# Kernel tuning notes

Measured on AMD Instinct MI355X. Metric: run time of the kernel, lower is better.

The kernel has to match this reference:

```python
import jax, jax.numpy as jnp
import numpy as np

B, N, M = 32, 65536, 64
IMG = 640.0
POS_THR, NEG_THR = 0.5, 0.4
ALPHA, GAMMA = 0.25, 2.0
BBOX_W = 2.0
EPS = 1e-6


def setup_inputs() -> dict:
    key = jax.random.key(0)
    k1, k2, k3, k4, k5 = jax.random.split(key, 5)
    # predictions: cx, cy in [0, IMG], w, h in [8, 72], obj logit ~ N(0,1)
    cxcy = jax.random.uniform(k1, (B, N, 2), jnp.float32) * IMG
    wh = jax.random.uniform(k2, (B, N, 2), jnp.float32) * 64.0 + 8.0
    obj = jax.random.normal(k3, (B, N, 1), jnp.float32)
    predictions = jnp.concatenate([cxcy, wh, obj], axis=-1)  # [B, N, 5]
    # ground-truth boxes in xyxy, centers in [0, IMG], sizes in [10, 100]
    gcxcy = jax.random.uniform(k4, (B, M, 2), jnp.float32) * IMG
    gwh = jax.random.uniform(k5, (B, M, 2), jnp.float32) * 90.0 + 10.0
    gt_boxes = jnp.concatenate([gcxcy - gwh / 2, gcxcy + gwh / 2], axis=-1)  # [B, M, 4]
    return {"predictions": predictions, "gt_boxes": gt_boxes}


def _focal(logits, targets):
    # stable BCE-with-logits, then focal modulation
    bce = jnp.maximum(logits, 0.0) - logits * targets + jnp.log1p(jnp.exp(-jnp.abs(logits)))
    p = jax.nn.sigmoid(logits)
    p_t = jnp.where(targets == 1.0, p, 1.0 - p)
    alpha_t = jnp.where(targets == 1.0, ALPHA, 1.0 - ALPHA)
    return alpha_t * (1.0 - p_t) ** GAMMA * bce


def _pairwise_iou(pb, gb):
    # pb: [N,4] xyxy, gb: [M,4] xyxy -> [N,M]
    x1 = jnp.maximum(pb[:, None, 0], gb[None, :, 0])
    y1 = jnp.maximum(pb[:, None, 1], gb[None, :, 1])
    x2 = jnp.minimum(pb[:, None, 2], gb[None, :, 2])
    y2 = jnp.minimum(pb[:, None, 3], gb[None, :, 3])
    inter = jnp.clip(x2 - x1, 0.0) * jnp.clip(y2 - y1, 0.0)
    area_p = (pb[:, 2] - pb[:, 0]) * (pb[:, 3] - pb[:, 1])
    area_g = (gb[:, 2] - gb[:, 0]) * (gb[:, 3] - gb[:, 1])
    union = area_p[:, None] + area_g[None, :] - inter
    return inter / jnp.clip(union, EPS)


def _giou_term(pb, gb):
    # elementwise 1 - GIoU; pb, gb: [N,4]
    x1 = jnp.maximum(pb[:, 0], gb[:, 0]); y1 = jnp.maximum(pb[:, 1], gb[:, 1])
    x2 = jnp.minimum(pb[:, 2], gb[:, 2]); y2 = jnp.minimum(pb[:, 3], gb[:, 3])
    inter = jnp.clip(x2 - x1, 0.0) * jnp.clip(y2 - y1, 0.0)
    area_p = (pb[:, 2] - pb[:, 0]) * (pb[:, 3] - pb[:, 1])
    area_g = (gb[:, 2] - gb[:, 0]) * (gb[:, 3] - gb[:, 1])
    union = area_p + area_g - inter
    iou = inter / jnp.clip(union, EPS)
    ex1 = jnp.minimum(pb[:, 0], gb[:, 0]); ey1 = jnp.minimum(pb[:, 1], gb[:, 1])
    ex2 = jnp.maximum(pb[:, 2], gb[:, 2]); ey2 = jnp.maximum(pb[:, 3], gb[:, 3])
    enc = (ex2 - ex1) * (ey2 - ey1)
    giou = iou - (enc - union) / jnp.clip(enc, EPS)
    return 1.0 - giou


def _per_image(pred, gt):
    # pred: [N,5] (cx,cy,w,h,obj), gt: [M,4] xyxy
    cx, cy, w, h = pred[:, 0], pred[:, 1], pred[:, 2], pred[:, 3]
    pb = jnp.stack([cx - w / 2, cy - h / 2, cx + w / 2, cy + h / 2], axis=1)  # decode to xyxy
    obj = pred[:, 4]
    ious = _pairwise_iou(pb, gt)  # [N, M]
    best_pred_per_gt = ious.max(axis=0)              # [M]
    best_pred_idx = jnp.argmax(ious, axis=0)         # [M]
    best_gt_per_pred = ious.max(axis=1)              # [N]
    best_gt_idx = jnp.argmax(ious, axis=1)           # [N]
    # force-match each GT's best anchor if its IoU > 0.1 (scatter-max)
    pos_scatter = jnp.zeros((pred.shape[0],), jnp.int32).at[best_pred_idx].max(
        (best_pred_per_gt > 0.1).astype(jnp.int32))
    pos = (pos_scatter > 0) | (best_gt_per_pred > POS_THR)
    neg = best_gt_per_pred < NEG_THR
    valid = pos | neg
    t = pos.astype(jnp.float32)
    fl = _focal(obj, t)
    vcnt = valid.sum().astype(jnp.float32)
    cls_loss = jnp.where(vcnt > 0, (fl * valid).sum() / jnp.maximum(vcnt, 1.0), 0.0)
    matched = gt[best_gt_idx]                        # [N,4]
    gterm = _giou_term(pb, matched)                  # [N]
    pcnt = pos.sum().astype(jnp.float32)
    reg_loss = jnp.where(pcnt > 0, (gterm * pos).sum() / jnp.maximum(pcnt, 1.0), 0.0)
    return cls_loss, reg_loss, pos.sum()


def reference(predictions, gt_boxes):
    cls_b, reg_b, npos_b = jax.vmap(_per_image)(predictions, gt_boxes)
    num_pos = jnp.maximum(npos_b.sum(), 1).astype(jnp.float32)
    bsz = jnp.float32(predictions.shape[0])
    total_cls = cls_b.sum() / bsz
    total_reg = reg_b.sum() / num_pos * bsz
    return total_cls + BBOX_W * total_reg
```

## Files before the change

### kernel.cpp

```cpp
#include <hip/hip_runtime.h>

#define NB 32
#define NPRED 65536
#define NGT 64
#define BLK 256
#define SLICES 32
#define CPB (NPRED / (SLICES * BLK))
#define NXB 32
#define BIN_SCALE 0.05f

#define POS_THR 0.5f
#define NEG_THR 0.4f
#define SCAT_THR 0.1f
#define EPSF 1e-6f


__device__ __forceinline__ int binidx(float x) {
    int bi = (int)(x * BIN_SCALE);
    return max(0, min(NXB - 1, bi));
}

__device__ __forceinline__ float focal_shared(float l, bool pos) {
    float e  = expf(-fabsf(l));
    float lg = log1pf(e);
    float rp = 1.f / (1.f + e);
    float p  = (l >= 0.f) ? rp : (1.f - rp);
    if (pos) { float q = 1.f - p; return 0.25f * q * q * ((fmaxf(l, 0.f) - l) + lg); }
    return 0.75f * p * p * (fmaxf(l, 0.f) + lg);
}

__device__ __forceinline__ float giou_term(float px1, float py1, float px2, float py2,
                                           float gx1, float gy1, float gx2, float gy2) {
    float x1 = fmaxf(px1, gx1), y1 = fmaxf(py1, gy1);
    float x2 = fminf(px2, gx2), y2 = fminf(py2, gy2);
    float dx = fmaxf(__fsub_rn(x2, x1), 0.f);
    float dy = fmaxf(__fsub_rn(y2, y1), 0.f);
    float inter = __fmul_rn(dx, dy);
    float ap = __fmul_rn(__fsub_rn(px2, px1), __fsub_rn(py2, py1));
    float ag = __fmul_rn(__fsub_rn(gx2, gx1), __fsub_rn(gy2, gy1));
    float uni = __fsub_rn(__fadd_rn(ap, ag), inter);
    float iou = __fdiv_rn(inter, fmaxf(uni, EPSF));
    float ex1 = fminf(px1, gx1), ey1 = fminf(py1, gy1);
    float ex2 = fmaxf(px2, gx2), ey2 = fmaxf(py2, gy2);
    float enc = __fmul_rn(__fsub_rn(ex2, ex1), __fsub_rn(ey2, ey1));
    float giou = __fsub_rn(iou, __fdiv_rn(__fsub_rn(enc, uni), fmaxf(enc, EPSF)));
    return __fsub_rn(1.f, giou);
}


__global__ __launch_bounds__(BLK) void passA(
    const float* __restrict__ pred, const float* __restrict__ gt,
    unsigned long long* __restrict__ keys,
    double* __restrict__ S_fl, double* __restrict__ S_gt,
    int* __restrict__ vcnt, int* __restrict__ pcnt)
{
    const int b = blockIdx.y;
    const int slice = blockIdx.x;
    const int tid = threadIdx.x;

    __shared__ float4 spred4[(BLK * 5) / 4];
    __shared__ float sgx1[NGT], sgy1[NGT], sgx2[NGT], sgy2[NGT], sgar[NGT];
    __shared__ unsigned long long skey[NGT];
    __shared__ unsigned long long binx[NXB], biny[NXB];
    __shared__ float rfl[BLK / 64], rgt[BLK / 64];
    __shared__ int rvp[BLK / 64];

    const float* base = pred + (size_t)b * NPRED * 5 + (size_t)slice * (CPB * BLK) * 5;

    const float4* src0 = (const float4*)base;
    float4 r0 = src0[tid];
    float4 r1;
    if (tid < 64) r1 = src0[BLK + tid];

    const float4* gtb = (const float4*)(gt + (size_t)b * NGT * 4);
    float4 gmine;
    if (tid < NGT) gmine = gtb[tid];
    if (tid < NXB) { binx[tid] = 0ULL; biny[tid] = 0ULL; }
    if (tid < NGT) {
        sgx1[tid] = gmine.x; sgy1[tid] = gmine.y;
        sgx2[tid] = gmine.z; sgy2[tid] = gmine.w;
        sgar[tid] = __fmul_rn(__fsub_rn(gmine.z, gmine.x), __fsub_rn(gmine.w, gmine.y));
        skey[tid] = 0ULL;
    }
    __syncthreads();
    if (tid < NGT) {
        unsigned long long bit = 1ULL << tid;
        int b1 = binidx(gmine.x), b2 = binidx(gmine.z);
        #pragma unroll
        for (int i = 0; i < 6; ++i) { int bb = min(b1 + i, NXB - 1); if (b1 + i <= b2) atomicOr(&binx[bb], bit); }
        b1 = binidx(gmine.y); b2 = binidx(gmine.w);
        #pragma unroll
        for (int i = 0; i < 6; ++i) { int bb = min(b1 + i, NXB - 1); if (b1 + i <= b2) atomicOr(&biny[bb], bit); }
    }

    float acc_fl = 0.f, acc_gt = 0.f;
    int acc_vp = 0;

    for (int c = 0; c < CPB; ++c) {
        __syncthreads();
        spred4[tid] = r0;
        if (tid < 64) spred4[BLK + tid] = r1;
        __syncthreads();
        if (c + 1 < CPB) {
            const float4* srcn = (const float4*)(base + (size_t)(c + 1) * BLK * 5);
            r0 = srcn[tid];
            if (tid < 64) r1 = srcn[BLK + tid];
        }

        const float* sp = (const float*)spred4;
        const float cx  = sp[tid * 5 + 0];
        const float cy  = sp[tid * 5 + 1];
        const float w   = sp[tid * 5 + 2];
        const float h   = sp[tid * 5 + 3];
        const float obj = sp[tid * 5 + 4];

        const float px1 = __fsub_rn(cx, __fmul_rn(w, 0.5f));
        const float py1 = __fsub_rn(cy, __fmul_rn(h, 0.5f));
        const float px2 = __fadd_rn(cx, __fmul_rn(w, 0.5f));
        const float py2 = __fadd_rn(cy, __fmul_rn(h, 0.5f));
        const float area_p = __fmul_rn(__fsub_rn(px2, px1), __fsub_rn(py2, py1));

        unsigned long long mx = 0ULL, my = 0ULL;
        {
            int b1 = binidx(px1), b2 = binidx(px2);
            #pragma unroll
            for (int i = 0; i < 5; ++i) { unsigned long long v = binx[min(b1 + i, NXB - 1)]; if (b1 + i <= b2) mx |= v; }
            b1 = binidx(py1); b2 = binidx(py2);
            #pragma unroll
            for (int i = 0; i < 5; ++i) { unsigned long long v = biny[min(b1 + i, NXB - 1)]; if (b1 + i <= b2) my |= v; }
        }
        unsigned long long m = mx & my;

        const unsigned n = (unsigned)(slice * (CPB * BLK) + c * BLK + tid);
        const unsigned long long nkey = (unsigned long long)(~n);

        float best_iou = 0.f;
        int best_j = 0;
        while (m) {
            int j0 = __ffsll(m) - 1; m &= m - 1;
            int j1 = -1;
            if (m) { j1 = __ffsll(m) - 1; m &= m - 1; }
            int j1c = (j1 >= 0) ? j1 : j0;
            float ax1 = sgx1[j0], ay1 = sgy1[j0], ax2 = sgx2[j0], ay2 = sgy2[j0], aga = sgar[j0];
            float bx1 = sgx1[j1c], by1 = sgy1[j1c], bx2 = sgx2[j1c], by2 = sgy2[j1c], agb = sgar[j1c];
            {
                float x1 = fmaxf(px1, ax1), y1 = fmaxf(py1, ay1);
                float x2 = fminf(px2, ax2), y2 = fminf(py2, ay2);
                float dx = fmaxf(__fsub_rn(x2, x1), 0.f);
                float dy = fmaxf(__fsub_rn(y2, y1), 0.f);
                float inter = __fmul_rn(dx, dy);
                if (inter > 0.f) {
                    float uni = __fsub_rn(__fadd_rn(area_p, aga), inter);
                    float iou = __fdiv_rn(inter, fmaxf(uni, EPSF));
                    if (iou > best_iou) { best_iou = iou; best_j = j0; }
                    atomicMax(&skey[j0], (((unsigned long long)__float_as_uint(iou)) << 32) | nkey);
                }
            }
            if (j1 >= 0) {
                float x1 = fmaxf(px1, bx1), y1 = fmaxf(py1, by1);
                float x2 = fminf(px2, bx2), y2 = fminf(py2, by2);
                float dx = fmaxf(__fsub_rn(x2, x1), 0.f);
                float dy = fmaxf(__fsub_rn(y2, y1), 0.f);
                float inter = __fmul_rn(dx, dy);
                if (inter > 0.f) {
                    float uni = __fsub_rn(__fadd_rn(area_p, agb), inter);
                    float iou = __fdiv_rn(inter, fmaxf(uni, EPSF));
                    if (iou > best_iou) { best_iou = iou; best_j = j1; }
                    atomicMax(&skey[j1], (((unsigned long long)__float_as_uint(iou)) << 32) | nkey);
                }
            }
        }

        const bool pos0   = best_iou > POS_THR;
        const bool negf   = best_iou < NEG_THR;
        const bool valid0 = pos0 || negf;
        if (valid0) acc_fl += focal_shared(obj, pos0);
        if (pos0) {
            acc_gt += giou_term(px1, py1, px2, py2,
                                sgx1[best_j], sgy1[best_j], sgx2[best_j], sgy2[best_j]);
        }
        acc_vp += (valid0 ? 1 : 0) | (pos0 ? 0x10000 : 0);
    }

    for (int off = 32; off; off >>= 1) {
        acc_fl += __shfl_down(acc_fl, off);
        acc_gt += __shfl_down(acc_gt, off);
        acc_vp += __shfl_down(acc_vp, off);
    }
    int wid = tid >> 6;
    if ((tid & 63) == 0) { rfl[wid] = acc_fl; rgt[wid] = acc_gt; rvp[wid] = acc_vp; }
    __syncthreads();
    if (tid == 0) {
        float sfl = 0.f, sgt2 = 0.f; int svp = 0;
        #pragma unroll
        for (int i = 0; i < BLK / 64; ++i) { sfl += rfl[i]; sgt2 += rgt[i]; svp += rvp[i]; }
        atomicAdd(&S_fl[b], (double)sfl);
        atomicAdd(&S_gt[b], (double)sgt2);
        atomicAdd(&vcnt[b], svp & 0xFFFF);
        atomicAdd(&pcnt[b], svp >> 16);
    }
    if (tid < NGT) {
        unsigned long long k = skey[tid];
        if (k) atomicMax(&keys[b * NGT + tid], k);
    }
}


__global__ __launch_bounds__(64) void passBC(
    const float* __restrict__ pred, const float* __restrict__ gt,
    const unsigned long long* __restrict__ keys,
    const double* __restrict__ S_fl, const double* __restrict__ S_gt,
    const int* __restrict__ vcnt, const int* __restrict__ pcnt,
    float* __restrict__ cls_b, float* __restrict__ reg_b, int* __restrict__ npos_b,
    unsigned* __restrict__ done, float* __restrict__ out)
{
    const int b = blockIdx.x;
    const int lane = threadIdx.x;

    __shared__ float4 sgt[NGT];
    __shared__ unsigned cn_list[NGT];

    const float4* gtb = (const float4*)(gt + (size_t)b * NGT * 4);
    float4 gj = gtb[lane];
    sgt[lane] = gj;

    unsigned long long key = keys[b * NGT + lane];
    float miou = __uint_as_float((unsigned)(key >> 32));
    unsigned n = ~((unsigned)(key & 0xFFFFFFFFULL));
    bool qual = miou > SCAT_THR;

    bool unique = qual;
    for (int j2 = 0; j2 < NGT; ++j2) {
        unsigned bn = __shfl(n, j2);
        int bq = __shfl((int)qual, j2);
        if (bq && j2 < lane && bn == n) unique = false;
    }
    unsigned long long mask = __ballot(unique ? 1 : 0);
    int NC = __popcll(mask);
    int slot = __popcll(mask & ((1ULL << lane) - 1ULL));
    if (unique) cn_list[slot] = n;
    __syncthreads();

    float cx = 0.f, cy = 0.f, w = 0.f, h = 0.f, obj = 0.f;
    if (lane < NC) {
        const float* p = pred + (size_t)b * NPRED * 5 + (size_t)cn_list[lane] * 5;
        cx = p[0]; cy = p[1]; w = p[2]; h = p[3]; obj = p[4];
    }
    float px1 = __fsub_rn(cx, __fmul_rn(w, 0.5f));
    float py1 = __fsub_rn(cy, __fmul_rn(h, 0.5f));
    float px2 = __fadd_rn(cx, __fmul_rn(w, 0.5f));
    float py2 = __fadd_rn(cy, __fmul_rn(h, 0.5f));
    float area_p = __fmul_rn(__fsub_rn(px2, px1), __fsub_rn(py2, py1));

    float bv = 0.f; int bj = 0;
    #pragma unroll 4
    for (int j = 0; j < NGT; ++j) {
        float4 g = sgt[j];
        float x1 = fmaxf(px1, g.x), y1 = fmaxf(py1, g.y);
        float x2 = fminf(px2, g.z), y2 = fminf(py2, g.w);
        float dx = fmaxf(__fsub_rn(x2, x1), 0.f);
        float dy = fmaxf(__fsub_rn(y2, y1), 0.f);
        float inter = __fmul_rn(dx, dy);
        if (inter > 0.f) {
            float ag = __fmul_rn(__fsub_rn(g.z, g.x), __fsub_rn(g.w, g.y));
            float uni = __fsub_rn(__fadd_rn(area_p, ag), inter);
            float iou = __fdiv_rn(inter, fmaxf(uni, EPSF));
            if (iou > bv) { bv = iou; bj = j; }
        }
    }

    double add_fl = 0.0, add_gt = 0.0;
    int add_v = 0, add_p = 0;
    if (lane < NC && !(bv > POS_THR)) {
        bool was_neg = bv < NEG_THR;
        float f1 = focal_shared(obj, true);
        float f0 = focal_shared(obj, false);
        add_fl = (double)f1 - (was_neg ? (double)f0 : 0.0);
        add_v = was_neg ? 0 : 1;
        add_p = 1;
        float4 gb = sgt[bj];
        add_gt = (double)giou_term(px1, py1, px2, py2, gb.x, gb.y, gb.z, gb.w);
    }

    for (int off = 32; off; off >>= 1) {
        add_fl += __shfl_down(add_fl, off);
        add_gt += __shfl_down(add_gt, off);
        add_v  += __shfl_down(add_v, off);
        add_p  += __shfl_down(add_p, off);
    }

    if (lane == 0) {
        double sfl = S_fl[b] + add_fl;
        double sgt2 = S_gt[b] + add_gt;
        int v = vcnt[b] + add_v;
        int pc = pcnt[b] + add_p;
        cls_b[b] = (v > 0) ? (float)(sfl / (double)(v > 1 ? v : 1)) : 0.f;
        reg_b[b] = (pc > 0) ? (float)(sgt2 / (double)(pc > 1 ? pc : 1)) : 0.f;
        npos_b[b] = pc;
    }

    __threadfence();
    unsigned t = 0;
    if (lane == 0) t = atomicAdd(done, 1u);
    t = __shfl(t, 0);
    if (t == NB - 1) {
        __threadfence();
        volatile float* vc = cls_b;
        volatile float* vr = reg_b;
        volatile int*   vn = npos_b;
        float cv = (lane < NB) ? vc[lane] : 0.f;
        float rv = (lane < NB) ? vr[lane] : 0.f;
        int   nv = (lane < NB) ? vn[lane] : 0;
        for (int off = 32; off; off >>= 1) {
            cv += __shfl_down(cv, off);
            rv += __shfl_down(rv, off);
            nv += __shfl_down(nv, off);
        }
        if (lane == 0) {
            float num_pos = fmaxf((float)nv, 1.f);
            out[0] = cv / (float)NB + 2.0f * (rv / num_pos * (float)NB);
        }
    }
}


extern "C" void kernel_launch(void* const* d_in, const int* in_sizes, int n_in,
                              void* d_out, int out_size, void* d_ws, size_t ws_size,
                              hipStream_t stream) {
    const float* pred = (const float*)d_in[0];
    const float* gt   = (const float*)d_in[1];
    float* out = (float*)d_out;

    char* ws = (char*)d_ws;
    unsigned long long* keys = (unsigned long long*)(ws + 0);
    double* S_fl   = (double*)(ws + 16384);
    double* S_gt   = (double*)(ws + 16640);
    int* vcnt      = (int*)(ws + 16896);
    int* pcnt      = (int*)(ws + 17024);
    float* cls_b   = (float*)(ws + 17152);
    float* reg_b   = (float*)(ws + 17280);
    int* npos_b    = (int*)(ws + 17408);
    unsigned* done = (unsigned*)(ws + 17536);

    hipMemsetAsync(d_ws, 0, 17664, stream);

    dim3 gridA(SLICES, NB);
    passA<<<gridA, BLK, 0, stream>>>(pred, gt, keys, S_fl, S_gt, vcnt, pcnt);
    passBC<<<NB, 64, 0, stream>>>(pred, gt, keys, S_fl, S_gt, vcnt, pcnt,
                                  cls_b, reg_b, npos_b, done, out);
}
```

Before: 126.0 us.

## Load four predictions per thread from registers and filter scatter atomics

Drops the shared-memory staging loop: each thread now reads five float4 values directly from global memory and handles four consecutive predictions unrolled in registers. The slice count doubles so the grid still covers all predictions, with more blocks in flight. The shared-memory atomicMax for the per-GT best anchor is now skipped when IoU is at or below the 0.1 force-match threshold, which cuts LDS atomic traffic. In exchange, each thread's loads are strided rather than coalesced across the wave, and register pressure rises from holding four predictions at once.

```diff
diff --git a/kernel.cpp b/kernel.cpp
--- a/kernel.cpp
+++ b/kernel.cpp
@@ -4,8 +4,8 @@
 #define NPRED 65536
 #define NGT 64
 #define BLK 256
-#define SLICES 32
-#define CPB (NPRED / (SLICES * BLK))
+#define SLICES 64
+#define PPT 4
 #define NXB 32
 #define BIN_SCALE 0.05f
 
@@ -58,19 +58,16 @@
     const int slice = blockIdx.x;
     const int tid = threadIdx.x;
 
-    __shared__ float4 spred4[(BLK * 5) / 4];
     __shared__ float sgx1[NGT], sgy1[NGT], sgx2[NGT], sgy2[NGT], sgar[NGT];
     __shared__ unsigned long long skey[NGT];
     __shared__ unsigned long long binx[NXB], biny[NXB];
     __shared__ float rfl[BLK / 64], rgt[BLK / 64];
     __shared__ int rvp[BLK / 64];
 
-    const float* base = pred + (size_t)b * NPRED * 5 + (size_t)slice * (CPB * BLK) * 5;
-
-    const float4* src0 = (const float4*)base;
-    float4 r0 = src0[tid];
-    float4 r1;
-    if (tid < 64) r1 = src0[BLK + tid];
+    const unsigned base_n = (unsigned)(slice * (BLK * PPT));
+    const float4* src4 = (const float4*)(pred + (size_t)b * NPRED * 5 + (size_t)base_n * 5)
+                         + (size_t)tid * 5;
+    float4 q0 = src4[0], q1 = src4[1], q2 = src4[2], q3 = src4[3], q4 = src4[4];
 
     const float4* gtb = (const float4*)(gt + (size_t)b * NGT * 4);
     float4 gmine;
@@ -92,46 +89,37 @@
         #pragma unroll
         for (int i = 0; i < 6; ++i) { int bb = min(b1 + i, NXB - 1); if (b1 + i <= b2) atomicOr(&biny[bb], bit); }
     }
+    __syncthreads();
+
+    const float cxa[PPT] = {q0.x, q1.y, q2.z, q3.w};
+    const float cya[PPT] = {q0.y, q1.z, q2.w, q4.x};
+    const float wa [PPT] = {q0.z, q1.w, q3.x, q4.y};
+    const float ha [PPT] = {q0.w, q2.x, q3.y, q4.z};
+    const float oba[PPT] = {q1.x, q2.y, q3.z, q4.w};
 
     float acc_fl = 0.f, acc_gt = 0.f;
     int acc_vp = 0;
 
-    for (int c = 0; c < CPB; ++c) {
-        __syncthreads();
-        spred4[tid] = r0;
-        if (tid < 64) spred4[BLK + tid] = r1;
-        __syncthreads();
-        if (c + 1 < CPB) {
-            const float4* srcn = (const float4*)(base + (size_t)(c + 1) * BLK * 5);
-            r0 = srcn[tid];
-            if (tid < 64) r1 = srcn[BLK + tid];
-        }
-
-        const float* sp = (const float*)spred4;
-        const float cx  = sp[tid * 5 + 0];
-        const float cy  = sp[tid * 5 + 1];
-        const float w   = sp[tid * 5 + 2];
-        const float h   = sp[tid * 5 + 3];
-        const float obj = sp[tid * 5 + 4];
-
-        const float px1 = __fsub_rn(cx, __fmul_rn(w, 0.5f));
-        const float py1 = __fsub_rn(cy, __fmul_rn(h, 0.5f));
-        const float px2 = __fadd_rn(cx, __fmul_rn(w, 0.5f));
-        const float py2 = __fadd_rn(cy, __fmul_rn(h, 0.5f));
+    #pragma unroll
+    for (int i = 0; i < PPT; ++i) {
+        const float px1 = __fsub_rn(cxa[i], __fmul_rn(wa[i], 0.5f));
+        const float py1 = __fsub_rn(cya[i], __fmul_rn(ha[i], 0.5f));
+        const float px2 = __fadd_rn(cxa[i], __fmul_rn(wa[i], 0.5f));
+        const float py2 = __fadd_rn(cya[i], __fmul_rn(ha[i], 0.5f));
         const float area_p = __fmul_rn(__fsub_rn(px2, px1), __fsub_rn(py2, py1));
 
         unsigned long long mx = 0ULL, my = 0ULL;
         {
             int b1 = binidx(px1), b2 = binidx(px2);
             #pragma unroll
-            for (int i = 0; i < 5; ++i) { unsigned long long v = binx[min(b1 + i, NXB - 1)]; if (b1 + i <= b2) mx |= v; }
+            for (int k = 0; k < 5; ++k) { unsigned long long v = binx[min(b1 + k, NXB - 1)]; if (b1 + k <= b2) mx |= v; }
             b1 = binidx(py1); b2 = binidx(py2);
             #pragma unroll
-            for (int i = 0; i < 5; ++i) { unsigned long long v = biny[min(b1 + i, NXB - 1)]; if (b1 + i <= b2) my |= v; }
+            for (int k = 0; k < 5; ++k) { unsigned long long v = biny[min(b1 + k, NXB - 1)]; if (b1 + k <= b2) my |= v; }
         }
         unsigned long long m = mx & my;
 
-        const unsigned n = (unsigned)(slice * (CPB * BLK) + c * BLK + tid);
+        const unsigned n = base_n + (unsigned)(PPT * tid + i);
         const unsigned long long nkey = (unsigned long long)(~n);
 
         float best_iou = 0.f;
@@ -153,7 +141,8 @@
                     float uni = __fsub_rn(__fadd_rn(area_p, aga), inter);
                     float iou = __fdiv_rn(inter, fmaxf(uni, EPSF));
                     if (iou > best_iou) { best_iou = iou; best_j = j0; }
-                    atomicMax(&skey[j0], (((unsigned long long)__float_as_uint(iou)) << 32) | nkey);
+                    if (iou > SCAT_THR)
+                        atomicMax(&skey[j0], (((unsigned long long)__float_as_uint(iou)) << 32) | nkey);
                 }
             }
             if (j1 >= 0) {
@@ -166,7 +155,8 @@
                     float uni = __fsub_rn(__fadd_rn(area_p, agb), inter);
                     float iou = __fdiv_rn(inter, fmaxf(uni, EPSF));
                     if (iou > best_iou) { best_iou = iou; best_j = j1; }
-                    atomicMax(&skey[j1], (((unsigned long long)__float_as_uint(iou)) << 32) | nkey);
+                    if (iou > SCAT_THR)
+                        atomicMax(&skey[j1], (((unsigned long long)__float_as_uint(iou)) << 32) | nkey);
                 }
             }
         }
@@ -174,7 +164,7 @@
         const bool pos0   = best_iou > POS_THR;
         const bool negf   = best_iou < NEG_THR;
         const bool valid0 = pos0 || negf;
-        if (valid0) acc_fl += focal_shared(obj, pos0);
+        if (valid0) acc_fl += focal_shared(oba[i], pos0);
         if (pos0) {
             acc_gt += giou_term(px1, py1, px2, py2,
                                 sgx1[best_j], sgy1[best_j], sgx2[best_j], sgy2[best_j]);
```

After: 123.6 us. Within noise of the previous version (-1.9%).
